# Performance work log

Measured on AMD Instinct MI355X. Metric: run time of the kernel, lower is better.

## Reference

```python
import jax, jax.numpy as jnp
import numpy as np

B, S, D, H, FF = 2, 2048, 1024, 16, 4096
DH = D // H
EPS = 1e-5


def _linear_params(key, din, dout):
    kw, kb = jax.random.split(key)
    lim = 1.0 / np.sqrt(din)
    W = jax.random.uniform(kw, (din, dout), jnp.float32, -lim, lim)
    b = jax.random.uniform(kb, (dout,), jnp.float32, -lim, lim)
    return W, b


def setup_inputs() -> dict:
    key = jax.random.key(0)
    ks = jax.random.split(key, 8)
    x = jax.random.normal(ks[0], (B, S, D), jnp.float32)
    mask = jnp.ones((B, 1, 1, S), jnp.int32)
    wq, bq = _linear_params(ks[1], D, D)
    wk, bk = _linear_params(ks[2], D, D)
    wv, bv = _linear_params(ks[3], D, D)
    w1, b1 = _linear_params(ks[4], D, D)       # linear1 (attn output proj)
    fw1, fb1 = _linear_params(ks[5], D, FF)    # ffn.w_1
    fw2, fb2 = _linear_params(ks[6], FF, D)    # ffn.w_2
    g1 = jnp.ones((D,), jnp.float32); be1 = jnp.zeros((D,), jnp.float32)
    g2 = jnp.ones((D,), jnp.float32); be2 = jnp.zeros((D,), jnp.float32)
    return dict(x=x, mask=mask, wq=wq, bq=bq, wk=wk, bk=bk, wv=wv, bv=bv,
                w1=w1, b1=b1, g1=g1, be1=be1,
                fw1=fw1, fb1=fb1, fw2=fw2, fb2=fb2, g2=g2, be2=be2)


def _layernorm(x, g, b):
    mu = jnp.mean(x, axis=-1, keepdims=True)
    var = jnp.mean(jnp.square(x - mu), axis=-1, keepdims=True)
    return (x - mu) * jax.lax.rsqrt(var + EPS) * g + b


def _encoder(x, mask, wq, bq, wk, bk, wv, bv, w1, b1, g1, be1,
             fw1, fb1, fw2, fb2, g2, be2):
    res = x
    # QKV projections, reshape to [B, H, S, DH]
    q = (x @ wq + bq).reshape(B, S, H, DH).transpose(0, 2, 1, 3)
    k = (x @ wk + bk).reshape(B, S, H, DH).transpose(0, 2, 1, 3)
    v = (x @ wv + bv).reshape(B, S, H, DH).transpose(0, 2, 1, 3)
    scores = jnp.einsum('bhqd,bhkd->bhqk', q, k) / np.sqrt(DH).astype(np.float32)
    scores = jnp.where(mask == 0, jnp.float32(-1e9), scores)
    probs = jax.nn.softmax(scores, axis=-1)  # dropout = identity in eval
    attn = jnp.einsum('bhqk,bhkd->bhqd', probs, v)
    attn = attn.transpose(0, 2, 1, 3).reshape(B, S, D)
    x = _layernorm(attn @ w1 + b1 + res, g1, be1)
    res = x
    ff = jax.nn.relu(x @ fw1 + fb1) @ fw2 + fb2
    return _layernorm(ff + res, g2, be2)


def reference(x, mask, wq, bq, wk, bk, wv, bv, w1, b1, g1, be1,
              fw1, fb1, fw2, fb2, g2, be2):
    return _encoder(x, mask, wq, bq, wk, bk, wv, bv, w1, b1, g1, be1,
                    fw1, fb1, fw2, fb2, g2, be2)
```

## Files before the change

### kernel.cpp

```cpp
#include <hip/hip_runtime.h>
#include <hip/hip_bf16.h>
#include <cstdint>

typedef unsigned short u16;
typedef __attribute__((ext_vector_type(8))) short bf16x8;
typedef __attribute__((ext_vector_type(4))) float f32x4;

#define DEVFN static __device__ __forceinline__

static constexpr int S   = 2048;
static constexpr int D   = 1024;
static constexpr int DHd = 64;
static constexpr int FFd = 4096;
static constexpr int M   = 4096;
static constexpr int LDQ = 3072;

static constexpr float SC2 = 0.18033688f;

DEVFN u16 f2b(float v) {
    union { __hip_bfloat16 h; u16 u; } x;
    x.h = __float2bfloat16(v);
    return x.u;
}

typedef const uint32_t __attribute__((address_space(1)))* gptr_t;
typedef uint32_t __attribute__((address_space(3)))* lptr_t;
DEVFN void load16(const void* g, void* l) {
    __builtin_amdgcn_global_load_lds((gptr_t)g, (lptr_t)l, 16, 0, 0);
}

template<int MODE>
__global__ __launch_bounds__(256, 3)
void gemm_bf16(const u16* __restrict__ A, const u16* __restrict__ BT,
               const float* __restrict__ bias, void* __restrict__ outp,
               int N, int K)
{
    __shared__ __align__(16) u16 As[128 * 64];
    __shared__ __align__(16) u16 Bs[128 * 64];
    const int tid  = threadIdx.x;
    const int lane = tid & 63;
    const int w    = tid >> 6;
    const int wm = w >> 1, wn = w & 1;
    const int g = lane >> 4, c = lane & 15;
    const int bn0 = blockIdx.x * 128;
    const int bm0 = blockIdx.y * 128;
    const int srow = tid >> 3;
    const int scol = (tid & 7) * 8;

    const f32x4 fz = {0.f, 0.f, 0.f, 0.f};
    f32x4 acc[4][4];
#pragma unroll
    for (int i = 0; i < 4; ++i)
#pragma unroll
        for (int j = 0; j < 4; ++j) acc[i][j] = fz;

    const u16* Ab = A  + (size_t)(bm0 + srow) * K + scol;
    const u16* Bb = BT + (size_t)(bn0 + srow) * K + scol;
    char* AsB = (char*)As + (size_t)tid * 16;
    char* BsB = (char*)Bs + (size_t)tid * 16;

    const int nk = K >> 6;
    for (int kt = 0; kt < nk; ++kt) {
        const int k0 = kt << 6;
        __syncthreads();
#pragma unroll
        for (int cc = 0; cc < 4; ++cc) {
            load16(Ab + (size_t)(cc * 32) * K + k0, AsB + cc * 4096);
            load16(Bb + (size_t)(cc * 32) * K + k0, BsB + cc * 4096);
        }
        __syncthreads();
#pragma unroll
        for (int kk = 0; kk < 2; ++kk) {
            bf16x8 af[4], bfv[4];
#pragma unroll
            for (int i = 0; i < 4; ++i)
                af[i] = *(const bf16x8*)&As[(wm*64 + i*16 + c) * 64 + kk*32 + g*8];
#pragma unroll
            for (int j = 0; j < 4; ++j)
                bfv[j] = *(const bf16x8*)&Bs[(wn*64 + j*16 + c) * 64 + kk*32 + g*8];
#pragma unroll
            for (int i = 0; i < 4; ++i)
#pragma unroll
                for (int j = 0; j < 4; ++j)
                    acc[i][j] = __builtin_amdgcn_mfma_f32_16x16x32_bf16(
                        af[i], bfv[j], acc[i][j], 0, 0, 0);
        }
    }

#pragma unroll
    for (int i = 0; i < 4; ++i) {
        const int row = bm0 + wm*64 + i*16 + g*4;
#pragma unroll
        for (int j = 0; j < 4; ++j) {
            const int col = bn0 + wn*64 + j*16 + c;
            const float bv = bias[col];
            const float sc = (MODE == 3 && col < D) ? SC2 : 1.f;
#pragma unroll
            for (int r = 0; r < 4; ++r) {
                float v = (acc[i][j][r] + bv) * sc;
                const size_t idx = (size_t)(row + r) * N + col;
                if (MODE == 2) {
                    ((u16*)outp)[idx] = f2b(v > 0.f ? v : 0.f);
                } else {
                    ((u16*)outp)[idx] = f2b(v);
                }
            }
        }
    }
}

template<int KTOT>
__global__ __launch_bounds__(256, 3)
void gemm_splitk(const u16* __restrict__ A, const u16* __restrict__ BT,
                 float* __restrict__ part)
{
    __shared__ __align__(16) u16 As[128 * 64];
    __shared__ __align__(16) u16 Bs[128 * 64];
    const int tid  = threadIdx.x;
    const int lane = tid & 63;
    const int w    = tid >> 6;
    const int wm = w >> 1, wn = w & 1;
    const int g = lane >> 4, c = lane & 15;
    const int bn0 = blockIdx.x * 128;
    const int bm0 = blockIdx.y * 128;
    const int z   = blockIdx.z;
    const int srow = tid >> 3;
    const int scol = (tid & 7) * 8;

    const f32x4 fz = {0.f, 0.f, 0.f, 0.f};
    f32x4 acc[4][4];
#pragma unroll
    for (int i = 0; i < 4; ++i)
#pragma unroll
        for (int j = 0; j < 4; ++j) acc[i][j] = fz;

    const u16* Ab = A  + (size_t)(bm0 + srow) * KTOT + z * (KTOT/2) + scol;
    const u16* Bb = BT + (size_t)(bn0 + srow) * KTOT + z * (KTOT/2) + scol;
    char* AsB = (char*)As + (size_t)tid * 16;
    char* BsB = (char*)Bs + (size_t)tid * 16;

    for (int kt = 0; kt < KTOT/128; ++kt) {
        const int k0 = kt << 6;
        __syncthreads();
#pragma unroll
        for (int cc = 0; cc < 4; ++cc) {
            load16(Ab + (size_t)(cc * 32) * KTOT + k0, AsB + cc * 4096);
            load16(Bb + (size_t)(cc * 32) * KTOT + k0, BsB + cc * 4096);
        }
        __syncthreads();
#pragma unroll
        for (int kk = 0; kk < 2; ++kk) {
            bf16x8 af[4], bfv[4];
#pragma unroll
            for (int i = 0; i < 4; ++i)
                af[i] = *(const bf16x8*)&As[(wm*64 + i*16 + c) * 64 + kk*32 + g*8];
#pragma unroll
            for (int j = 0; j < 4; ++j)
                bfv[j] = *(const bf16x8*)&Bs[(wn*64 + j*16 + c) * 64 + kk*32 + g*8];
#pragma unroll
            for (int i = 0; i < 4; ++i)
#pragma unroll
                for (int j = 0; j < 4; ++j)
                    acc[i][j] = __builtin_amdgcn_mfma_f32_16x16x32_bf16(
                        af[i], bfv[j], acc[i][j], 0, 0, 0);
        }
    }

    float* outz = part + (size_t)z * M * D;
#pragma unroll
    for (int i = 0; i < 4; ++i) {
        const int row = bm0 + wm*64 + i*16 + g*4;
#pragma unroll
        for (int j = 0; j < 4; ++j) {
            const int col = bn0 + wn*64 + j*16 + c;
#pragma unroll
            for (int r = 0; r < 4; ++r)
                outz[(size_t)(row + r) * D + col] = acc[i][j][r];
        }
    }
}

__global__ __launch_bounds__(256)
void ln_part_fused(const float* __restrict__ part, const float* __restrict__ bias,
                   const float* __restrict__ resid, const float* __restrict__ gam,
                   const float* __restrict__ bet, u16* __restrict__ out_b,
                   float* __restrict__ out_f)
{
    const int row = blockIdx.x;
    const int tid = threadIdx.x;
    __shared__ float red1[4], red2[4];
    const float4 p0 = ((const float4*)(part + (size_t)row * D))[tid];
    const float4 p1 = ((const float4*)(part + (size_t)(M + row) * D))[tid];
    const float4 bv = ((const float4*)bias)[tid];
    const float4 rv = ((const float4*)(resid + (size_t)row * D))[tid];
    const float y0 = p0.x + p1.x + bv.x + rv.x;
    const float y1 = p0.y + p1.y + bv.y + rv.y;
    const float y2 = p0.z + p1.z + bv.z + rv.z;
    const float y3 = p0.w + p1.w + bv.w + rv.w;
    float s1 = y0 + y1 + y2 + y3;
#pragma unroll
    for (int off = 1; off < 64; off <<= 1) s1 += __shfl_xor(s1, off);
    if ((tid & 63) == 0) red1[tid >> 6] = s1;
    __syncthreads();
    const float mu = (red1[0] + red1[1] + red1[2] + red1[3]) * (1.f / 1024.f);
    const float d0 = y0 - mu, d1 = y1 - mu, d2 = y2 - mu, d3 = y3 - mu;
    float s2 = d0*d0 + d1*d1 + d2*d2 + d3*d3;
#pragma unroll
    for (int off = 1; off < 64; off <<= 1) s2 += __shfl_xor(s2, off);
    if ((tid & 63) == 0) red2[tid >> 6] = s2;
    __syncthreads();
    const float var = (red2[0] + red2[1] + red2[2] + red2[3]) * (1.f / 1024.f);
    const float rs = rsqrtf(var + 1e-5f);
    const int c0 = tid * 4;
    const float o0 = d0 * rs * gam[c0+0] + bet[c0+0];
    const float o1 = d1 * rs * gam[c0+1] + bet[c0+1];
    const float o2 = d2 * rs * gam[c0+2] + bet[c0+2];
    const float o3 = d3 * rs * gam[c0+3] + bet[c0+3];
    if (out_b) {
        union { u16 u[4]; uint2 v; } pk;
        pk.u[0] = f2b(o0); pk.u[1] = f2b(o1); pk.u[2] = f2b(o2); pk.u[3] = f2b(o3);
        ((uint2*)(out_b + (size_t)row * D))[tid] = pk.v;
    }
    if (out_f) {
        float4 yv; yv.x = o0; yv.y = o1; yv.z = o2; yv.w = o3;
        ((float4*)(out_f + (size_t)row * D))[tid] = yv;
    }
}

__global__ __launch_bounds__(256, 3)
void attn_fwd9(const u16* __restrict__ QKV, const u16* __restrict__ VT,
               u16* __restrict__ Ob)
{
    __shared__ __align__(16) u16 Ks[3][64 * 64];
    __shared__ __align__(16) u16 Vs[3][64 * 64];
    __shared__ __align__(16) u16 Ps[4][32 * 72];
    const int tid  = threadIdx.x;
    const int lane = tid & 63;
    const int w    = tid >> 6;
    const int g = lane >> 4, c = lane & 15;
    const int bh = blockIdx.y;
    const int b = bh >> 4, h = bh & 15;
    const int q0 = blockIdx.x * 128 + w * 32;

    const u16* Qb = QKV;
    const u16* Kb = QKV + 1024;

    bf16x8 aq[2][2];
#pragma unroll
    for (int rt = 0; rt < 2; ++rt)
#pragma unroll
        for (int kk = 0; kk < 2; ++kk)
            aq[rt][kk] = *(const bf16x8*)&Qb[(size_t)(b*S + q0 + rt*16 + c) * LDQ
                                             + h*DHd + kk*32 + g*8];

    const f32x4 fz = {0.f, 0.f, 0.f, 0.f};
    const short one_b = (short)0x3F80;
    const bf16x8 onesv = {one_b, one_b, one_b, one_b, one_b, one_b, one_b, one_b};
    f32x4 o[2][4];
    f32x4 ol[2];
#pragma unroll
    for (int rt = 0; rt < 2; ++rt) {
        ol[rt] = fz;
#pragma unroll
        for (int j = 0; j < 4; ++j) o[rt][j] = fz;
    }

    const int sr = tid >> 3;
    const int glog = (tid & 7) ^ (sr & 7);
    const u16* Ksrc = Kb + (size_t)(b*S + sr) * LDQ + h*DHd + glog*8;
    const u16* Vsrc = VT + (size_t)(bh*DHd + sr) * S + glog*8;
    char* Kd0 = (char*)&Ks[0][0] + (size_t)tid * 16;
    char* Vd0 = (char*)&Vs[0][0] + (size_t)tid * 16;

#define STAGE(BUFI, kt_)                                                        \
    {                                                                           \
        const int kr0_ = (kt_) * 64;                                            \
        _Pragma("unroll")                                                       \
        for (int cc = 0; cc < 2; ++cc) {                                        \
            load16(Ksrc + (size_t)(kr0_ + cc*32) * LDQ, Kd0 + (BUFI)*8192 + cc*4096); \
            load16(Vsrc + (size_t)(cc*32) * S + kr0_,   Vd0 + (BUFI)*8192 + cc*4096); \
        }                                                                       \
    }
#define WAITBAR(N)                                                              \
    {                                                                           \
        asm volatile("s_waitcnt vmcnt(" #N ")" ::: "memory");                   \
        __builtin_amdgcn_s_barrier();                                           \
        __builtin_amdgcn_sched_barrier(0);                                      \
    }

    u16* pw = &Ps[w][0];
    const int c7 = c & 7;

    auto tile_body = [&](const u16* K0, const u16* V0) {
        bf16x8 bk[4][2];
#pragma unroll
        for (int j = 0; j < 4; ++j)
#pragma unroll
            for (int kk = 0; kk < 2; ++kk)
                bk[j][kk] = *(const bf16x8*)&K0[(j*16 + c) * 64 + (((kk<<2)+g) ^ c7) * 8];

#pragma unroll
        for (int rt = 0; rt < 2; ++rt) {
            f32x4 sv[4];
            __builtin_amdgcn_s_setprio(1);
#pragma unroll
            for (int j = 0; j < 4; ++j) {
                sv[j] = fz;
#pragma unroll
                for (int kk = 0; kk < 2; ++kk)
                    sv[j] = __builtin_amdgcn_mfma_f32_16x16x32_bf16(
                        bk[j][kk], aq[rt][kk], sv[j], 0, 0, 0);
            }
            __builtin_amdgcn_s_setprio(0);

#pragma unroll
            for (int j = 0; j < 4; ++j) {
                const float p0 = exp2f(sv[j][0]);
                const float p1 = exp2f(sv[j][1]);
                const float p2 = exp2f(sv[j][2]);
                const float p3 = exp2f(sv[j][3]);
                union { u16 u[4]; uint2 v; } pk;
                pk.u[0] = f2b(p0); pk.u[1] = f2b(p1);
                pk.u[2] = f2b(p2); pk.u[3] = f2b(p3);
                *(uint2*)&pw[(rt*16 + c) * 72 + j*16 + g*4] = pk.v;
            }
        }

        __builtin_amdgcn_s_setprio(1);
#pragma unroll
        for (int st = 0; st < 2; ++st) {
            bf16x8 bv[4];
#pragma unroll
            for (int j = 0; j < 4; ++j)
                bv[j] = *(const bf16x8*)&V0[(j*16 + c) * 64 + (((st<<2)+g) ^ c7) * 8];
#pragma unroll
            for (int rt = 0; rt < 2; ++rt) {
                const bf16x8 ap = *(const bf16x8*)&pw[(rt*16 + c) * 72 + st*32 + g*8];
#pragma unroll
                for (int j = 0; j < 4; ++j)
                    o[rt][j] = __builtin_amdgcn_mfma_f32_16x16x32_bf16(
                        ap, bv[j], o[rt][j], 0, 0, 0);
                ol[rt] = __builtin_amdgcn_mfma_f32_16x16x32_bf16(
                    ap, onesv, ol[rt], 0, 0, 0);
            }
        }
        __builtin_amdgcn_s_setprio(0);
    };

    STAGE(0, 0);
    STAGE(1, 1);
    WAITBAR(4);

    int kt = 0;
#pragma unroll 1
    for (int it = 0; it < 10; ++it, kt += 3) {
        STAGE(2, kt + 2); tile_body(&Ks[0][0], &Vs[0][0]); WAITBAR(4);
        STAGE(0, kt + 3); tile_body(&Ks[1][0], &Vs[1][0]); WAITBAR(4);
        STAGE(1, kt + 4); tile_body(&Ks[2][0], &Vs[2][0]); WAITBAR(4);
    }
    tile_body(&Ks[0][0], &Vs[0][0]); WAITBAR(0);
    tile_body(&Ks[1][0], &Vs[1][0]);
#undef STAGE
#undef WAITBAR

#pragma unroll
    for (int rt = 0; rt < 2; ++rt) {
#pragma unroll
        for (int r = 0; r < 4; ++r) {
            const float rl = __builtin_amdgcn_rcpf(ol[rt][r]);
            const size_t row = (size_t)(b*S + q0 + rt*16 + 4*g + r) * D + h*DHd;
#pragma unroll
            for (int j = 0; j < 4; ++j)
                Ob[row + j*16 + c] = f2b(o[rt][j][r] * rl);
        }
    }
}

__global__ void cast_bf16_k(const float* __restrict__ in, u16* __restrict__ out) {
    const int i = blockIdx.x * blockDim.x + threadIdx.x;
    const float4 v = ((const float4*)in)[i];
    union { u16 u[4]; uint2 p; } pk;
    pk.u[0] = f2b(v.x); pk.u[1] = f2b(v.y); pk.u[2] = f2b(v.z); pk.u[3] = f2b(v.w);
    ((uint2*)out)[i] = pk.p;
}

__global__ void concat3_k(const float* __restrict__ a, const float* __restrict__ b,
                          const float* __restrict__ c, float* __restrict__ o) {
    const int i = blockIdx.x * blockDim.x + threadIdx.x;
    o[i] = i < 1024 ? a[i] : (i < 2048 ? b[i - 1024] : c[i - 2048]);
}

__global__ void transpose_cast_k(const float* __restrict__ src, u16* __restrict__ dst,
                                 int R, int C) {
    __shared__ float tile[32][33];
    const int c0 = blockIdx.x * 32, r0 = blockIdx.y * 32;
    const int tx = threadIdx.x, ty = threadIdx.y;
#pragma unroll
    for (int i = 0; i < 4; ++i)
        tile[ty + i*8][tx] = src[(size_t)(r0 + ty + i*8) * C + c0 + tx];
    __syncthreads();
#pragma unroll
    for (int i = 0; i < 4; ++i)
        dst[(size_t)(c0 + ty + i*8) * R + r0 + tx] = f2b(tile[tx][ty + i*8]);
}

__global__ __launch_bounds__(256)
void v_transpose_k(const u16* __restrict__ Vp, u16* __restrict__ VT) {
    __shared__ u16 tile[64][65];
    const int bh = blockIdx.y, b = bh >> 4, h = bh & 15;
    const int s0 = blockIdx.x * 64;
    const int tid = threadIdx.x;
#pragma unroll
    for (int i = 0; i < 16; ++i) {
        const int e = tid + i * 256, r = e >> 6, cc = e & 63;
        tile[r][cc] = Vp[(size_t)(b*S + s0 + r) * LDQ + h*DHd + cc];
    }
    __syncthreads();
#pragma unroll
    for (int i = 0; i < 16; ++i) {
        const int e = tid + i * 256, d = e >> 6, sc = e & 63;
        VT[(size_t)(bh*DHd + d) * S + s0 + sc] = tile[sc][d];
    }
}

extern "C" void kernel_launch(void* const* d_in, const int* in_sizes, int n_in,
                              void* d_out, int out_size, void* d_ws, size_t ws_size,
                              hipStream_t stream)
{
    (void)in_sizes; (void)n_in; (void)out_size; (void)ws_size;
    const float* x   = (const float*)d_in[0];
    const float* wq  = (const float*)d_in[2];
    const float* bq  = (const float*)d_in[3];
    const float* wk  = (const float*)d_in[4];
    const float* bk  = (const float*)d_in[5];
    const float* wv  = (const float*)d_in[6];
    const float* bv  = (const float*)d_in[7];
    const float* w1  = (const float*)d_in[8];
    const float* b1  = (const float*)d_in[9];
    const float* g1  = (const float*)d_in[10];
    const float* be1 = (const float*)d_in[11];
    const float* fw1 = (const float*)d_in[12];
    const float* fb1 = (const float*)d_in[13];
    const float* fw2 = (const float*)d_in[14];
    const float* fb2 = (const float*)d_in[15];
    const float* g2  = (const float*)d_in[16];
    const float* be2 = (const float*)d_in[17];

    char* ws = (char*)d_ws;
    size_t off = 0;
    auto alloc = [&](size_t bytes) -> void* {
        void* p = ws + off;
        off += (bytes + 255) & ~(size_t)255;
        return p;
    };
    u16*   Xb    = (u16*)alloc((size_t)M * D * 2);
    u16*   WqkvT = (u16*)alloc((size_t)3 * D * D * 2);
    u16*   W1T   = (u16*)alloc((size_t)D * D * 2);
    u16*   F1T   = (u16*)alloc((size_t)D * FFd * 2);
    u16*   F2T   = (u16*)alloc((size_t)D * FFd * 2);
    u16*   QKV   = (u16*)alloc((size_t)M * LDQ * 2);
    u16*   VTh   = (u16*)alloc((size_t)M * D * 2);
    u16*   Ob    = (u16*)alloc((size_t)M * D * 2);
    float* x1f   = (float*)alloc((size_t)M * D * 4);
    u16*   x1b   = (u16*)alloc((size_t)M * D * 2);
    u16*   Hb    = (u16*)alloc((size_t)M * FFd * 2);
    float* bqkv  = (float*)alloc((size_t)LDQ * 4);

    float* Part = (float*)QKV;

    cast_bf16_k<<<dim3(M * D / 1024), dim3(256), 0, stream>>>(x, Xb);
    dim3 tb(32, 8);
    transpose_cast_k<<<dim3(D/32, D/32),   tb, 0, stream>>>(wq,  WqkvT,                 D, D);
    transpose_cast_k<<<dim3(D/32, D/32),   tb, 0, stream>>>(wk,  WqkvT + (size_t)D*D,   D, D);
    transpose_cast_k<<<dim3(D/32, D/32),   tb, 0, stream>>>(wv,  WqkvT + (size_t)2*D*D, D, D);
    transpose_cast_k<<<dim3(D/32, D/32),   tb, 0, stream>>>(w1,  W1T, D, D);
    transpose_cast_k<<<dim3(FFd/32, D/32), tb, 0, stream>>>(fw1, F1T, D, FFd);
    transpose_cast_k<<<dim3(D/32, FFd/32), tb, 0, stream>>>(fw2, F2T, FFd, D);
    concat3_k<<<dim3(LDQ/256), dim3(256), 0, stream>>>(bq, bk, bv, bqkv);

    gemm_bf16<3><<<dim3(LDQ/128, M/128), 256, 0, stream>>>(Xb, WqkvT, bqkv, QKV, LDQ, D);

    v_transpose_k<<<dim3(S/64, 32), 256, 0, stream>>>(QKV + 2048, VTh);

    attn_fwd9<<<dim3(S/128, 32), 256, 0, stream>>>(QKV, VTh, Ob);

    gemm_splitk<D><<<dim3(D/128, M/128, 2), 256, 0, stream>>>(Ob, W1T, Part);

    ln_part_fused<<<dim3(M), 256, 0, stream>>>(Part, b1, x, g1, be1, x1b, x1f);

    gemm_bf16<2><<<dim3(FFd/128, M/128), 256, 0, stream>>>(x1b, F1T, fb1, Hb, FFd, D);

    gemm_splitk<FFd><<<dim3(D/128, M/128, 2), 256, 0, stream>>>(Hb, F2T, Part);

    ln_part_fused<<<dim3(M), 256, 0, stream>>>(Part, fb2, x1f, g2, be2, nullptr, (float*)d_out);
}
```

Measured before the change: 273.5 us.

## Replace 128x128 bf16 GEMM with 256x256 double-buffered swizzled LDS pipeline

Swaps the QKV and FFN-up GEMMs to a new 512-thread kernel with 256x256 output tiles. The kernel double-buffers A and B tiles in 128KB of LDS, applies an XOR swizzle to avoid bank conflicts, and interleaves the async global-to-LDS loads for the next k-step with MFMA work through split barriers and s_setprio. The aim is more data reuse per tile and better overlap of loads with MFMA compute. In exchange, the grid is much smaller (fewer blocks than CUs for QKV) and LDS pressure allows only one block per CU, so load balance and latency hiding could suffer.

```diff
diff --git a/kernel.cpp b/kernel.cpp
--- a/kernel.cpp
+++ b/kernel.cpp
@@ -30,80 +30,162 @@
 }
 
 template<int MODE>
-__global__ __launch_bounds__(256, 3)
-void gemm_bf16(const u16* __restrict__ A, const u16* __restrict__ BT,
-               const float* __restrict__ bias, void* __restrict__ outp,
-               int N, int K)
+__global__ __launch_bounds__(512, 2)
+void gemm256(const u16* __restrict__ A, const u16* __restrict__ BT,
+             const float* __restrict__ bias, u16* __restrict__ outp, int N)
 {
-    __shared__ __align__(16) u16 As[128 * 64];
-    __shared__ __align__(16) u16 Bs[128 * 64];
+    constexpr int K = 1024;
+    __shared__ __align__(16) u16 Lds[65536];
     const int tid  = threadIdx.x;
     const int lane = tid & 63;
     const int w    = tid >> 6;
-    const int wm = w >> 1, wn = w & 1;
+    const int wm = w >> 2, wn = w & 3;
     const int g = lane >> 4, c = lane & 15;
-    const int bn0 = blockIdx.x * 128;
-    const int bm0 = blockIdx.y * 128;
-    const int srow = tid >> 3;
-    const int scol = (tid & 7) * 8;
+    const int c7 = c & 7;
+    const int bn0 = blockIdx.x * 256;
+    const int bm0 = blockIdx.y * 256;
+
+    const int sr = tid >> 3;
+    const int gl = (tid & 7) ^ (sr & 7);
+    const u16* Asrc = A  + (size_t)(bm0 + sr) * K + gl * 8;
+    const u16* Bsrc = BT + (size_t)(bn0 + sr) * K + gl * 8;
+    char* dA = (char*)Lds + (size_t)tid * 16;
+    char* dB = dA + 32768;
+
+#define STG_A(BUF, H, KT)                                                       \
+    { _Pragma("unroll") for (int Lh = 0; Lh < 2; ++Lh)                          \
+        load16(Asrc + (size_t)((H)*128 + Lh*64) * K + (KT)*64,                  \
+               dA + (BUF)*65536 + (H)*16384 + Lh*8192); }
+#define STG_B(BUF, H, KT)                                                       \
+    { _Pragma("unroll") for (int Lh = 0; Lh < 2; ++Lh)                          \
+        load16(Bsrc + (size_t)((H)*128 + Lh*64) * K + (KT)*64,                  \
+               dB + (BUF)*65536 + (H)*16384 + Lh*8192); }
+#define VMCNT(N_) asm volatile("s_waitcnt vmcnt(" #N_ ")" ::: "memory")
+#define BAR() { __builtin_amdgcn_s_barrier(); __builtin_amdgcn_sched_barrier(0); }
+
+    const char* lbase = (const char*)Lds;
+    auto rdA = [&](int buf, int i, int kk) -> bf16x8 {
+        const int half = i >> 2;
+        const int lr = (2*(i & 3) + wm) * 16 + c;
+        return *(const bf16x8*)(lbase + buf*65536 + half*16384 + lr*128
+                                + (((kk<<2) + g) ^ c7) * 16);
+    };
+    auto rdB = [&](int buf, int j, int kk) -> bf16x8 {
+        const int half = j >> 1;
+        const int lr = (j & 1)*64 + wn*16 + c;
+        return *(const bf16x8*)(lbase + buf*65536 + 32768 + half*16384 + lr*128
+                                + (((kk<<2) + g) ^ c7) * 16);
+    };
 
     const f32x4 fz = {0.f, 0.f, 0.f, 0.f};
-    f32x4 acc[4][4];
-#pragma unroll
-    for (int i = 0; i < 4; ++i)
+    f32x4 acc[8][4];
+#pragma unroll
+    for (int i = 0; i < 8; ++i)
 #pragma unroll
         for (int j = 0; j < 4; ++j) acc[i][j] = fz;
 
-    const u16* Ab = A  + (size_t)(bm0 + srow) * K + scol;
-    const u16* Bb = BT + (size_t)(bn0 + srow) * K + scol;
-    char* AsB = (char*)As + (size_t)tid * 16;
-    char* BsB = (char*)Bs + (size_t)tid * 16;
-
-    const int nk = K >> 6;
-    for (int kt = 0; kt < nk; ++kt) {
-        const int k0 = kt << 6;
-        __syncthreads();
-#pragma unroll
-        for (int cc = 0; cc < 4; ++cc) {
-            load16(Ab + (size_t)(cc * 32) * K + k0, AsB + cc * 4096);
-            load16(Bb + (size_t)(cc * 32) * K + k0, BsB + cc * 4096);
-        }
-        __syncthreads();
-#pragma unroll
-        for (int kk = 0; kk < 2; ++kk) {
-            bf16x8 af[4], bfv[4];
-#pragma unroll
-            for (int i = 0; i < 4; ++i)
-                af[i] = *(const bf16x8*)&As[(wm*64 + i*16 + c) * 64 + kk*32 + g*8];
-#pragma unroll
-            for (int j = 0; j < 4; ++j)
-                bfv[j] = *(const bf16x8*)&Bs[(wn*64 + j*16 + c) * 64 + kk*32 + g*8];
-#pragma unroll
-            for (int i = 0; i < 4; ++i)
-#pragma unroll
-                for (int j = 0; j < 4; ++j)
+    bf16x8 af[4][2], bf[4][2];
+
+    auto body = [&](int cur, int nxt, int kt, bool stage) {
+        if (stage) STG_A(nxt, 0, kt + 1);
+#pragma unroll
+        for (int i = 0; i < 4; ++i)
+#pragma unroll
+            for (int kk = 0; kk < 2; ++kk) af[i][kk] = rdA(cur, i, kk);
+#pragma unroll
+        for (int j = 0; j < 2; ++j)
+#pragma unroll
+            for (int kk = 0; kk < 2; ++kk) bf[j][kk] = rdB(cur, j, kk);
+        __builtin_amdgcn_s_setprio(1);
+#pragma unroll
+        for (int i = 0; i < 4; ++i)
+#pragma unroll
+            for (int j = 0; j < 2; ++j)
+#pragma unroll
+                for (int kk = 0; kk < 2; ++kk)
                     acc[i][j] = __builtin_amdgcn_mfma_f32_16x16x32_bf16(
-                        af[i], bfv[j], acc[i][j], 0, 0, 0);
-        }
-    }
-
-#pragma unroll
-    for (int i = 0; i < 4; ++i) {
-        const int row = bm0 + wm*64 + i*16 + g*4;
+                        af[i][kk], bf[j][kk], acc[i][j], 0, 0, 0);
+        __builtin_amdgcn_s_setprio(0);
+        if (stage) { VMCNT(4); } else { VMCNT(2); }
+        BAR();
+        if (stage) STG_B(nxt, 0, kt + 1);
+#pragma unroll
+        for (int j = 2; j < 4; ++j)
+#pragma unroll
+            for (int kk = 0; kk < 2; ++kk) bf[j][kk] = rdB(cur, j, kk);
+        __builtin_amdgcn_s_setprio(1);
+#pragma unroll
+        for (int i = 0; i < 4; ++i)
+#pragma unroll
+            for (int j = 2; j < 4; ++j)
+#pragma unroll
+                for (int kk = 0; kk < 2; ++kk)
+                    acc[i][j] = __builtin_amdgcn_mfma_f32_16x16x32_bf16(
+                        af[i][kk], bf[j][kk], acc[i][j], 0, 0, 0);
+        __builtin_amdgcn_s_setprio(0);
+        if (stage) { VMCNT(4); } else { VMCNT(0); }
+        BAR();
+        if (stage) STG_B(nxt, 1, kt + 1);
+#pragma unroll
+        for (int i = 4; i < 8; ++i)
+#pragma unroll
+            for (int kk = 0; kk < 2; ++kk) af[i - 4][kk] = rdA(cur, i, kk);
+        __builtin_amdgcn_s_setprio(1);
+#pragma unroll
+        for (int i = 4; i < 8; ++i)
+#pragma unroll
+            for (int j = 0; j < 2; ++j)
+#pragma unroll
+                for (int kk = 0; kk < 2; ++kk)
+                    acc[i][j] = __builtin_amdgcn_mfma_f32_16x16x32_bf16(
+                        af[i - 4][kk], bf[j][kk], acc[i][j], 0, 0, 0);
+        __builtin_amdgcn_s_setprio(0);
+        if (stage) STG_A(nxt, 1, kt + 1);
+        __builtin_amdgcn_s_setprio(1);
+#pragma unroll
+        for (int i = 4; i < 8; ++i)
+#pragma unroll
+            for (int j = 2; j < 4; ++j)
+#pragma unroll
+                for (int kk = 0; kk < 2; ++kk)
+                    acc[i][j] = __builtin_amdgcn_mfma_f32_16x16x32_bf16(
+                        af[i - 4][kk], bf[j][kk], acc[i][j], 0, 0, 0);
+        __builtin_amdgcn_s_setprio(0);
+        if (stage) { VMCNT(4); BAR(); }
+    };
+
+    STG_A(0, 0, 0); STG_B(0, 0, 0); STG_B(0, 1, 0); STG_A(0, 1, 0);
+    VMCNT(4);
+    BAR();
+
+#pragma unroll 1
+    for (int kt = 0; kt < 14; kt += 2) {
+        body(0, 1, kt, true);
+        body(1, 0, kt + 1, true);
+    }
+    body(0, 1, 14, true);
+    body(1, 0, 15, false);
+#undef STG_A
+#undef STG_B
+#undef VMCNT
+#undef BAR
+
+#pragma unroll
+    for (int i = 0; i < 8; ++i) {
+        const int fm = (i >> 2) * 8 + (i & 3) * 2 + wm;
+        const int row = bm0 + fm * 16 + 4 * g;
 #pragma unroll
         for (int j = 0; j < 4; ++j) {
-            const int col = bn0 + wn*64 + j*16 + c;
+            const int fn = (j >> 1) * 8 + (j & 1) * 4 + wn;
+            const int col = bn0 + fn * 16 + c;
             const float bv = bias[col];
             const float sc = (MODE == 3 && col < D) ? SC2 : 1.f;
 #pragma unroll
             for (int r = 0; r < 4; ++r) {
-                float v = (acc[i][j][r] + bv) * sc;
-                const size_t idx = (size_t)(row + r) * N + col;
-                if (MODE == 2) {
-                    ((u16*)outp)[idx] = f2b(v > 0.f ? v : 0.f);
-                } else {
-                    ((u16*)outp)[idx] = f2b(v);
-                }
+                float v = acc[i][j][r] + bv;
+                if (MODE == 2) v = v > 0.f ? v : 0.f;
+                v *= sc;
+                outp[(size_t)(row + r) * N + col] = f2b(v);
             }
         }
     }
@@ -478,7 +560,7 @@
     transpose_cast_k<<<dim3(D/32, FFd/32), tb, 0, stream>>>(fw2, F2T, FFd, D);
     concat3_k<<<dim3(LDQ/256), dim3(256), 0, stream>>>(bq, bk, bv, bqkv);
 
-    gemm_bf16<3><<<dim3(LDQ/128, M/128), 256, 0, stream>>>(Xb, WqkvT, bqkv, QKV, LDQ, D);
+    gemm256<3><<<dim3(LDQ/256, M/256), 512, 0, stream>>>(Xb, WqkvT, bqkv, QKV, LDQ);
 
     v_transpose_k<<<dim3(S/64, 32), 256, 0, stream>>>(QKV + 2048, VTh);
 
@@ -488,7 +570,7 @@
 
     ln_part_fused<<<dim3(M), 256, 0, stream>>>(Part, b1, x, g1, be1, x1b, x1f);
 
-    gemm_bf16<2><<<dim3(FFd/128, M/128), 256, 0, stream>>>(x1b, F1T, fb1, Hb, FFd, D);
+    gemm256<2><<<dim3(FFd/256, M/256), 512, 0, stream>>>(x1b, F1T, fb1, Hb, FFd);
 
     gemm_splitk<FFd><<<dim3(D/128, M/128, 2), 256, 0, stream>>>(Hb, F2T, Part);
 
```

New measurement: 257.2 us. 1.06x faster.
